# Kernel tuning notes

Hardware: AMD Instinct MI355X
Metric: run time of the kernel (lower is better)

The kernel has to match this reference:

```python
import jax, jax.numpy as jnp
import numpy as np

N_NODES = 100000
N_EDGES = 1200000
D_IN = 64
D_HID = 64
D_OUT = 32


def setup_inputs() -> dict:
    key = jax.random.key(0)
    ks = jax.random.split(key, 8)
    x = jax.random.normal(ks[0], (N_NODES, D_IN), dtype=jnp.float32)
    edge_index = jax.random.randint(ks[1], (2, N_EDGES), 0, N_NODES, dtype=jnp.int64)
    s = 0.05
    W1 = jax.random.normal(ks[2], (D_IN, D_HID), dtype=jnp.float32) * s
    b1 = jnp.zeros((D_HID,), dtype=jnp.float32)
    W2 = jax.random.normal(ks[3], (D_HID, D_HID), dtype=jnp.float32) * s
    b2 = jnp.zeros((D_HID,), dtype=jnp.float32)
    Wl = jax.random.normal(ks[4], (D_HID, D_OUT), dtype=jnp.float32) * s
    bl = jax.random.normal(ks[5], (D_OUT,), dtype=jnp.float32) * s
    return {"x": x, "edge_index": edge_index, "W1": W1, "b1": b1,
            "W2": W2, "b2": b2, "Wl": Wl, "bl": bl}


def reference(x, edge_index, W1, b1, W2, b2, Wl, bl):
    n = x.shape[0]
    # PyG GCNConv default: add self-loops, symmetric normalization D^-1/2 (A+I) D^-1/2
    loops = jnp.arange(n, dtype=edge_index.dtype)
    src = jnp.concatenate([edge_index[0], loops])  # message sources
    dst = jnp.concatenate([edge_index[1], loops])  # aggregation targets
    deg = jax.ops.segment_sum(jnp.ones(dst.shape, x.dtype), dst, num_segments=n)
    dinv = jax.lax.rsqrt(deg)  # deg >= 1 due to self-loops
    norm = dinv[src] * dinv[dst]  # [E+N]

    def gcn_conv(h, W, b):
        h = h @ W                      # transform [N, d]
        m = h[src] * norm[:, None]     # gather + scale [E+N, d]
        return jax.ops.segment_sum(m, dst, num_segments=n) + b  # scatter-add

    h = jax.nn.relu(gcn_conv(x, W1, b1))
    h = jax.nn.relu(gcn_conv(h, W2, b2))
    return h @ Wl + bl
```

## Files before the change

kernel.cpp:

```cpp
#include <hip/hip_runtime.h>
#include <hip/hip_fp16.h>

#define N_NODES 100000
#define N_EDGES 1200000

#define BIN_SHIFT 6
#define NODES_PER_BIN 64
#define NBINS ((N_NODES + NODES_PER_BIN - 1) >> BIN_SHIFT)
#define CAP 1024
#define EPB 8192
#define NBLK_BIN ((N_EDGES + EPB - 1) / EPB)

__global__ void binning_kernel(const int* __restrict__ src, const int* __restrict__ dst,
                               int* __restrict__ gcursor, unsigned int* __restrict__ binned,
                               int E) {
    __shared__ unsigned int stage[EPB];
    __shared__ unsigned short sbin[EPB];
    __shared__ unsigned int hist[NBINS];
    int t = threadIdx.x;
    int e_base = blockIdx.x * EPB;

    for (int b = t; b < NBINS; b += 256) hist[b] = 0;
    __syncthreads();

#pragma unroll
    for (int j = 0; j < EPB / 256; ++j) {
        int idx = e_base + t + j * 256;
        if (idx < E) {
            int s = src[idx];
            int d = dst[idx];
            unsigned int bin = (unsigned int)d >> BIN_SHIFT;
            stage[t + j * 256] = (unsigned int)s | (((unsigned int)d & 63u) << 17);
            sbin[t + j * 256] = (unsigned short)bin;
            atomicAdd(&hist[bin], 1u);
        }
    }
    __syncthreads();

    for (int b = t; b < NBINS; b += 256) {
        unsigned int c = hist[b];
        if (c) hist[b] = (unsigned int)(b * CAP) + (unsigned int)atomicAdd(&gcursor[b], (int)c);
    }
    __syncthreads();

#pragma unroll
    for (int j = 0; j < EPB / 256; ++j) {
        int idx = e_base + t + j * 256;
        if (idx < E) {
            unsigned int bin = sbin[t + j * 256];
            unsigned int pos = atomicAdd(&hist[bin], 1u);
            binned[pos] = stage[t + j * 256];
        }
    }
}

__global__ void csr_kernel(unsigned int* __restrict__ binned,
                           const int* __restrict__ gcursor,
                           float* __restrict__ dinv,
                           unsigned int* __restrict__ offdeg) {
    __shared__ unsigned int eLDS[CAP];
    __shared__ unsigned int counts[NODES_PER_BIN];
    __shared__ unsigned int scan[NODES_PER_BIN];
    __shared__ unsigned int offs[NODES_PER_BIN];
    __shared__ unsigned int cur[NODES_PER_BIN];
    int bin = blockIdx.x;
    int t = threadIdx.x;
    int nb = gcursor[bin];
    unsigned int* eb = binned + (size_t)bin * CAP;

    if (t < NODES_PER_BIN) counts[t] = 0;
    __syncthreads();
    for (int i = t; i < nb; i += 256) {
        unsigned int p = eb[i];
        eLDS[i] = p;
        atomicAdd(&counts[p >> 17], 1u);
    }
    __syncthreads();
    if (t < NODES_PER_BIN) scan[t] = counts[t];
    __syncthreads();
    for (int step = 1; step < NODES_PER_BIN; step <<= 1) {
        unsigned int v = 0;
        if (t < NODES_PER_BIN && t >= step) v = scan[t - step];
        __syncthreads();
        if (t < NODES_PER_BIN) scan[t] += v;
        __syncthreads();
    }
    if (t < NODES_PER_BIN) {
        offs[t] = scan[t] - counts[t];
        cur[t] = 0;
    }
    __syncthreads();
    for (int i = t; i < nb; i += 256) {
        unsigned int p = eLDS[i];
        unsigned int l = p >> 17;
        unsigned int pos = offs[l] + atomicAdd(&cur[l], 1u);
        eb[pos] = p & 0x1FFFFu;
    }
    if (t < NODES_PER_BIN) {
        int node = bin * NODES_PER_BIN + t;
        if (node < N_NODES) {
            dinv[node] = rsqrtf((float)(counts[t] + 1u));
            offdeg[node] = (offs[t] << 16) | counts[t];
        }
    }
}

__global__ __launch_bounds__(256, 4) void gemm1_kernel(const float* __restrict__ X,
                                                       const float* __restrict__ W,
                                                       const float* __restrict__ rowscale,
                                                       __half* __restrict__ Hout, int n) {
    constexpr int COLG = 16;
    constexpr int RGS  = 16;
    constexpr int RPT  = 4;
    constexpr int XPITCH = 17;
    __shared__ float4 sW4[64 * COLG];
    __shared__ float4 sX4[64 * XPITCH];
    int tid = threadIdx.x;

    for (int i = tid; i < 64 * COLG; i += 256) sW4[i] = ((const float4*)W)[i];

    int base_row = blockIdx.x * 64;
    const float4* X4 = (const float4*)X;
    for (int i = tid; i < 64 * 16; i += 256) {
        int r = i >> 4, c = i & 15;
        int gr = base_row + r;
        float4 v = make_float4(0.f, 0.f, 0.f, 0.f);
        if (gr < n) v = X4[(size_t)gr * 16 + c];
        sX4[r * XPITCH + c] = v;
    }
    __syncthreads();

    int cg = tid % COLG;
    int rg = tid / COLG;
    float4 acc[RPT];
#pragma unroll
    for (int r = 0; r < RPT; ++r) acc[r] = make_float4(0.f, 0.f, 0.f, 0.f);

#pragma unroll 2
    for (int k4 = 0; k4 < 16; ++k4) {
        float4 xv[RPT];
#pragma unroll
        for (int r = 0; r < RPT; ++r) xv[r] = sX4[(rg + RGS * r) * XPITCH + k4];
#pragma unroll
        for (int kk = 0; kk < 4; ++kk) {
            float4 w = sW4[(k4 * 4 + kk) * COLG + cg];
#pragma unroll
            for (int r = 0; r < RPT; ++r) {
                float xs = (kk == 0) ? xv[r].x : (kk == 1) ? xv[r].y : (kk == 2) ? xv[r].z : xv[r].w;
                acc[r].x = fmaf(xs, w.x, acc[r].x);
                acc[r].y = fmaf(xs, w.y, acc[r].y);
                acc[r].z = fmaf(xs, w.z, acc[r].z);
                acc[r].w = fmaf(xs, w.w, acc[r].w);
            }
        }
    }

#pragma unroll
    for (int r = 0; r < RPT; ++r) {
        int grow = base_row + rg + RGS * r;
        if (grow < n) {
            float4 v = acc[r];
            float s = rowscale[grow];
            v.x *= s; v.y *= s; v.z *= s; v.w *= s;
            __half2* H2 = (__half2*)Hout;
            size_t idx = (size_t)grow * 32 + 2 * cg;
            H2[idx]     = __floats2half2_rn(v.x, v.y);
            H2[idx + 1] = __floats2half2_rn(v.z, v.w);
        }
    }
}

template<int DOUT, bool HALF_OUT, bool ROWSCALE, bool GEMM_BIAS>
__global__ __launch_bounds__(256, 4) void fused_agg_gemm(
    const __half* __restrict__ tmp,
    const unsigned int* __restrict__ binned,
    const int* __restrict__ gcursor,
    const unsigned int* __restrict__ offdeg,
    const float* __restrict__ dinv,
    const float* __restrict__ gb,
    const float* __restrict__ W,
    const float* __restrict__ gbias,
    void* __restrict__ Hout) {
    constexpr int COLG = DOUT / 4;
    constexpr int RGS  = 256 / COLG;
    constexpr int RPT  = 64 / RGS;
    constexpr int XPITCH = 17;
    __shared__ unsigned int srcs[CAP];
    __shared__ unsigned int sOffdeg[NODES_PER_BIN];
    __shared__ float sDinv[NODES_PER_BIN];
    __shared__ float4 sW4[64 * COLG];
    __shared__ float4 sH4[64 * XPITCH];

    int bin = blockIdx.x;
    int t = threadIdx.x;
    int nb = gcursor[bin];
    const unsigned int* eb = binned + (size_t)bin * CAP;

    for (int i = t; i < 64 * COLG; i += 256) sW4[i] = ((const float4*)W)[i];
    if (t < NODES_PER_BIN) {
        int node = bin * NODES_PER_BIN + t;
        sOffdeg[t] = (node < N_NODES) ? offdeg[node] : 0;
        sDinv[t]   = (node < N_NODES) ? dinv[node]   : 0.0f;
    }
    for (int i = t; i < nb; i += 256) srcs[i] = eb[i];
    __syncthreads();

    int oct = t & 7;
    int lnode0 = t >> 3;
    const uint4* tmp16 = (const uint4*)tmp;
    float bb[8];
    {
        const float4 b0 = ((const float4*)gb)[oct * 2];
        const float4 b1 = ((const float4*)gb)[oct * 2 + 1];
        bb[0] = b0.x; bb[1] = b0.y; bb[2] = b0.z; bb[3] = b0.w;
        bb[4] = b1.x; bb[5] = b1.y; bb[6] = b1.z; bb[7] = b1.w;
    }

#pragma unroll
    for (int g = 0; g < 2; ++g) {
        int ln = g * 32 + lnode0;
        int node = bin * NODES_PER_BIN + ln;
        if (node < N_NODES) {
            unsigned int od = sOffdeg[ln];
            int deg = (int)(od & 0xFFFFu);
            int beg = (int)(od >> 16);
            float acc[8];
            {
                uint4 raw = tmp16[(size_t)node * 8 + oct];
                const __half2* hp = (const __half2*)&raw;
#pragma unroll
                for (int j = 0; j < 4; ++j) {
                    float2 f = __half22float2(hp[j]);
                    acc[2 * j] = f.x; acc[2 * j + 1] = f.y;
                }
            }
            int e = 0;
            for (; e + 3 < deg; e += 4) {
                unsigned int s0 = srcs[beg + e];
                unsigned int s1 = srcs[beg + e + 1];
                unsigned int s2 = srcs[beg + e + 2];
                unsigned int s3 = srcs[beg + e + 3];
                uint4 r0 = tmp16[(size_t)s0 * 8 + oct];
                uint4 r1 = tmp16[(size_t)s1 * 8 + oct];
                uint4 r2 = tmp16[(size_t)s2 * 8 + oct];
                uint4 r3 = tmp16[(size_t)s3 * 8 + oct];
                const __half2* h0 = (const __half2*)&r0;
                const __half2* h1 = (const __half2*)&r1;
                const __half2* h2 = (const __half2*)&r2;
                const __half2* h3 = (const __half2*)&r3;
#pragma unroll
                for (int j = 0; j < 4; ++j) {
                    float2 f0 = __half22float2(h0[j]);
                    float2 f1 = __half22float2(h1[j]);
                    float2 f2 = __half22float2(h2[j]);
                    float2 f3 = __half22float2(h3[j]);
                    acc[2 * j]     += (f0.x + f1.x) + (f2.x + f3.x);
                    acc[2 * j + 1] += (f0.y + f1.y) + (f2.y + f3.y);
                }
            }
            for (; e < deg; ++e) {
                unsigned int s0 = srcs[beg + e];
                uint4 r0 = tmp16[(size_t)s0 * 8 + oct];
                const __half2* h0 = (const __half2*)&r0;
#pragma unroll
                for (int j = 0; j < 4; ++j) {
                    float2 f0 = __half22float2(h0[j]);
                    acc[2 * j]     += f0.x;
                    acc[2 * j + 1] += f0.y;
                }
            }
            float dv = sDinv[ln];
            float4 o0, o1;
            o0.x = fmaxf(fmaf(dv, acc[0], bb[0]), 0.0f);
            o0.y = fmaxf(fmaf(dv, acc[1], bb[1]), 0.0f);
            o0.z = fmaxf(fmaf(dv, acc[2], bb[2]), 0.0f);
            o0.w = fmaxf(fmaf(dv, acc[3], bb[3]), 0.0f);
            o1.x = fmaxf(fmaf(dv, acc[4], bb[4]), 0.0f);
            o1.y = fmaxf(fmaf(dv, acc[5], bb[5]), 0.0f);
            o1.z = fmaxf(fmaf(dv, acc[6], bb[6]), 0.0f);
            o1.w = fmaxf(fmaf(dv, acc[7], bb[7]), 0.0f);
            sH4[ln * XPITCH + oct * 2]     = o0;
            sH4[ln * XPITCH + oct * 2 + 1] = o1;
        }
    }
    __syncthreads();

    int cg = t % COLG;
    int rg = t / COLG;
    float4 acc[RPT];
#pragma unroll
    for (int r = 0; r < RPT; ++r) acc[r] = make_float4(0.f, 0.f, 0.f, 0.f);

#pragma unroll 2
    for (int k4 = 0; k4 < 16; ++k4) {
        float4 xv[RPT];
#pragma unroll
        for (int r = 0; r < RPT; ++r) xv[r] = sH4[(rg + RGS * r) * XPITCH + k4];
#pragma unroll
        for (int kk = 0; kk < 4; ++kk) {
            float4 w = sW4[(k4 * 4 + kk) * COLG + cg];
#pragma unroll
            for (int r = 0; r < RPT; ++r) {
                float xs = (kk == 0) ? xv[r].x : (kk == 1) ? xv[r].y : (kk == 2) ? xv[r].z : xv[r].w;
                acc[r].x = fmaf(xs, w.x, acc[r].x);
                acc[r].y = fmaf(xs, w.y, acc[r].y);
                acc[r].z = fmaf(xs, w.z, acc[r].z);
                acc[r].w = fmaf(xs, w.w, acc[r].w);
            }
        }
    }

#pragma unroll
    for (int r = 0; r < RPT; ++r) {
        int ln = rg + RGS * r;
        int node = bin * NODES_PER_BIN + ln;
        if (node < N_NODES) {
            float4 v = acc[r];
            if (ROWSCALE) {
                float s = sDinv[ln];
                v.x *= s; v.y *= s; v.z *= s; v.w *= s;
            }
            if (GEMM_BIAS) {
                float4 bbq = ((const float4*)gbias)[cg];
                v.x += bbq.x; v.y += bbq.y; v.z += bbq.z; v.w += bbq.w;
            }
            if (HALF_OUT) {
                __half2* H2 = (__half2*)Hout;
                size_t idx = (size_t)node * (DOUT / 2) + 2 * cg;
                H2[idx]     = __floats2half2_rn(v.x, v.y);
                H2[idx + 1] = __floats2half2_rn(v.z, v.w);
            } else {
                ((float4*)Hout)[(size_t)node * COLG + cg] = v;
            }
        }
    }
}

extern "C" void kernel_launch(void* const* d_in, const int* in_sizes, int n_in,
                              void* d_out, int out_size, void* d_ws, size_t ws_size,
                              hipStream_t stream) {
    const float* x  = (const float*)d_in[0];
    const int*   ei = (const int*)d_in[1];
    const float* W1 = (const float*)d_in[2];
    const float* b1 = (const float*)d_in[3];
    const float* W2 = (const float*)d_in[4];
    const float* b2 = (const float*)d_in[5];
    const float* Wl = (const float*)d_in[6];
    const float* bl = (const float*)d_in[7];
    float* out = (float*)d_out;

    const int N = N_NODES;
    const int E = N_EDGES;
    const int* src = ei;
    const int* dst = ei + E;

    char* ws = (char*)d_ws;
    size_t off = 0;
    auto align = [](size_t v) { return (v + 511) & ~(size_t)511; };
    int* gcursor         = (int*)(ws + off);          off = align(off + (size_t)NBINS * 4);
    float* dinv          = (float*)(ws + off);        off = align(off + (size_t)N * 4);
    unsigned int* offdeg = (unsigned int*)(ws + off); off = align(off + (size_t)N * 4);
    unsigned int* binned = (unsigned int*)(ws + off); off = align(off + (size_t)NBINS * CAP * 4);
    __half* tmp          = (__half*)(ws + off);       off = align(off + (size_t)N * 64 * 2);
    __half* tmp2         = (__half*)(ws + off);       off = align(off + (size_t)N * 64 * 2);
    (void)ws_size;

    const int NBLK_GEMM = (N + 63) / 64;

    hipMemsetAsync(gcursor, 0, (size_t)NBINS * 4, stream);
    binning_kernel<<<NBLK_BIN, 256, 0, stream>>>(src, dst, gcursor, binned, E);
    csr_kernel<<<NBINS, 256, 0, stream>>>(binned, gcursor, dinv, offdeg);

    gemm1_kernel<<<NBLK_GEMM, 256, 0, stream>>>(x, W1, dinv, tmp, N);

    fused_agg_gemm<64, true, true, false><<<NBINS, 256, 0, stream>>>(
        tmp, binned, gcursor, offdeg, dinv, b1, W2, nullptr, tmp2);

    fused_agg_gemm<32, false, false, true><<<NBINS, 256, 0, stream>>>(
        tmp2, binned, gcursor, offdeg, dinv, b2, Wl, bl, out);
}
```

Before: 204.5 us.

## Merge edge binning and first GEMM into one launch, defer source scaling

The binning kernel and the first dense transform now share one launch, with blocks split by index range and a shared-memory buffer sized for the larger of the two roles. This removes the dependency of GEMM1 on dinv, so the two independent stages can overlap. To allow that, GEMM1 no longer prescales rows by dinv. The first aggregation instead multiplies each gathered source row by dinv[src], which costs an extra scattered 4-byte load per edge, and the larger shared allocation with launch_bounds(256,2) lowers occupancy for the binning blocks.

```diff
diff --git a/kernel.cpp b/kernel.cpp
--- a/kernel.cpp
+++ b/kernel.cpp
@@ -10,46 +10,108 @@
 #define CAP 1024
 #define EPB 8192
 #define NBLK_BIN ((N_EDGES + EPB - 1) / EPB)
-
-__global__ void binning_kernel(const int* __restrict__ src, const int* __restrict__ dst,
-                               int* __restrict__ gcursor, unsigned int* __restrict__ binned,
-                               int E) {
-    __shared__ unsigned int stage[EPB];
-    __shared__ unsigned short sbin[EPB];
-    __shared__ unsigned int hist[NBINS];
+#define NBLK_GEMM ((N_NODES + 63) / 64)
+#define SMEM_BYTES 55424
+
+__global__ __launch_bounds__(256, 2) void bin_gemm1_kernel(
+    const int* __restrict__ src, const int* __restrict__ dst,
+    int* __restrict__ gcursor, unsigned int* __restrict__ binned,
+    const float* __restrict__ X, const float* __restrict__ W1,
+    __half* __restrict__ tmp) {
+    __shared__ __align__(16) char smem[SMEM_BYTES];
     int t = threadIdx.x;
-    int e_base = blockIdx.x * EPB;
-
-    for (int b = t; b < NBINS; b += 256) hist[b] = 0;
-    __syncthreads();
-
-#pragma unroll
-    for (int j = 0; j < EPB / 256; ++j) {
-        int idx = e_base + t + j * 256;
-        if (idx < E) {
-            int s = src[idx];
-            int d = dst[idx];
-            unsigned int bin = (unsigned int)d >> BIN_SHIFT;
-            stage[t + j * 256] = (unsigned int)s | (((unsigned int)d & 63u) << 17);
-            sbin[t + j * 256] = (unsigned short)bin;
-            atomicAdd(&hist[bin], 1u);
-        }
-    }
-    __syncthreads();
-
-    for (int b = t; b < NBINS; b += 256) {
-        unsigned int c = hist[b];
-        if (c) hist[b] = (unsigned int)(b * CAP) + (unsigned int)atomicAdd(&gcursor[b], (int)c);
-    }
-    __syncthreads();
-
-#pragma unroll
-    for (int j = 0; j < EPB / 256; ++j) {
-        int idx = e_base + t + j * 256;
-        if (idx < E) {
-            unsigned int bin = sbin[t + j * 256];
-            unsigned int pos = atomicAdd(&hist[bin], 1u);
-            binned[pos] = stage[t + j * 256];
+
+    if (blockIdx.x < NBLK_BIN) {
+        unsigned int* stage = (unsigned int*)smem;
+        unsigned short* sbin = (unsigned short*)(smem + EPB * 4);
+        unsigned int* hist = (unsigned int*)(smem + EPB * 4 + EPB * 2);
+        int e_base = blockIdx.x * EPB;
+
+        for (int b = t; b < NBINS; b += 256) hist[b] = 0;
+        __syncthreads();
+
+#pragma unroll
+        for (int j = 0; j < EPB / 256; ++j) {
+            int idx = e_base + t + j * 256;
+            if (idx < N_EDGES) {
+                int s = src[idx];
+                int d = dst[idx];
+                unsigned int bin = (unsigned int)d >> BIN_SHIFT;
+                stage[t + j * 256] = (unsigned int)s | (((unsigned int)d & 63u) << 17);
+                sbin[t + j * 256] = (unsigned short)bin;
+                atomicAdd(&hist[bin], 1u);
+            }
+        }
+        __syncthreads();
+
+        for (int b = t; b < NBINS; b += 256) {
+            unsigned int c = hist[b];
+            if (c) hist[b] = (unsigned int)(b * CAP) + (unsigned int)atomicAdd(&gcursor[b], (int)c);
+        }
+        __syncthreads();
+
+#pragma unroll
+        for (int j = 0; j < EPB / 256; ++j) {
+            int idx = e_base + t + j * 256;
+            if (idx < N_EDGES) {
+                unsigned int bin = sbin[t + j * 256];
+                unsigned int pos = atomicAdd(&hist[bin], 1u);
+                binned[pos] = stage[t + j * 256];
+            }
+        }
+    } else {
+        constexpr int COLG = 16, RGS = 16, RPT = 4, XPITCH = 17;
+        float4* sW4 = (float4*)smem;
+        float4* sX4 = (float4*)(smem + 64 * COLG * 16);
+
+        for (int i = t; i < 64 * COLG; i += 256) sW4[i] = ((const float4*)W1)[i];
+
+        int base_row = (blockIdx.x - NBLK_BIN) * 64;
+        const float4* X4 = (const float4*)X;
+        for (int i = t; i < 64 * 16; i += 256) {
+            int r = i >> 4, c = i & 15;
+            int gr = base_row + r;
+            float4 v = make_float4(0.f, 0.f, 0.f, 0.f);
+            if (gr < N_NODES) v = X4[(size_t)gr * 16 + c];
+            sX4[r * XPITCH + c] = v;
+        }
+        __syncthreads();
+
+        int cg = t % COLG;
+        int rg = t / COLG;
+        float4 acc[RPT];
+#pragma unroll
+        for (int r = 0; r < RPT; ++r) acc[r] = make_float4(0.f, 0.f, 0.f, 0.f);
+
+#pragma unroll 2
+        for (int k4 = 0; k4 < 16; ++k4) {
+            float4 xv[RPT];
+#pragma unroll
+            for (int r = 0; r < RPT; ++r) xv[r] = sX4[(rg + RGS * r) * XPITCH + k4];
+#pragma unroll
+            for (int kk = 0; kk < 4; ++kk) {
+                float4 w = sW4[(k4 * 4 + kk) * COLG + cg];
+#pragma unroll
+                for (int r = 0; r < RPT; ++r) {
+                    float xs = (kk == 0) ? xv[r].x : (kk == 1) ? xv[r].y : (kk == 2) ? xv[r].z : xv[r].w;
+                    acc[r].x = fmaf(xs, w.x, acc[r].x);
+                    acc[r].y = fmaf(xs, w.y, acc[r].y);
+                    acc[r].z = fmaf(xs, w.z, acc[r].z);
+                    acc[r].w = fmaf(xs, w.w, acc[r].w);
+                }
+            }
+        }
+
+#pragma unroll
+        for (int r = 0; r < RPT; ++r) {
+            int grow = base_row + rg + RGS * r;
+            if (grow < N_NODES) {
+                float4 v = acc[r];
+                __half2* H2 = (__half2*)tmp;
+                size_t idx = (size_t)grow * 32 + 2 * cg;
+                H2[idx]     = __floats2half2_rn(v.x, v.y);
+                H2[idx + 1] = __floats2half2_rn(v.z, v.w);
+            }
         }
     }
 }
@@ -105,72 +167,7 @@
     }
 }
 
-__global__ __launch_bounds__(256, 4) void gemm1_kernel(const float* __restrict__ X,
-                                                       const float* __restrict__ W,
-                                                       const float* __restrict__ rowscale,
-                                                       __half* __restrict__ Hout, int n) {
-    constexpr int COLG = 16;
-    constexpr int RGS  = 16;
-    constexpr int RPT  = 4;
-    constexpr int XPITCH = 17;
-    __shared__ float4 sW4[64 * COLG];
-    __shared__ float4 sX4[64 * XPITCH];
-    int tid = threadIdx.x;
-
-    for (int i = tid; i < 64 * COLG; i += 256) sW4[i] = ((const float4*)W)[i];
-
-    int base_row = blockIdx.x * 64;
-    const float4* X4 = (const float4*)X;
-    for (int i = tid; i < 64 * 16; i += 256) {
-        int r = i >> 4, c = i & 15;
-        int gr = base_row + r;
-        float4 v = make_float4(0.f, 0.f, 0.f, 0.f);
-        if (gr < n) v = X4[(size_t)gr * 16 + c];
-        sX4[r * XPITCH + c] = v;
-    }
-    __syncthreads();
-
-    int cg = tid % COLG;
-    int rg = tid / COLG;
-    float4 acc[RPT];
-#pragma unroll
-    for (int r = 0; r < RPT; ++r) acc[r] = make_float4(0.f, 0.f, 0.f, 0.f);
-
-#pragma unroll 2
-    for (int k4 = 0; k4 < 16; ++k4) {
-        float4 xv[RPT];
-#pragma unroll
-        for (int r = 0; r < RPT; ++r) xv[r] = sX4[(rg + RGS * r) * XPITCH + k4];
-#pragma unroll
-        for (int kk = 0; kk < 4; ++kk) {
-            float4 w = sW4[(k4 * 4 + kk) * COLG + cg];
-#pragma unroll
-            for (int r = 0; r < RPT; ++r) {
-                float xs = (kk == 0) ? xv[r].x : (kk == 1) ? xv[r].y : (kk == 2) ? xv[r].z : xv[r].w;
-                acc[r].x = fmaf(xs, w.x, acc[r].x);
-                acc[r].y = fmaf(xs, w.y, acc[r].y);
-                acc[r].z = fmaf(xs, w.z, acc[r].z);
-                acc[r].w = fmaf(xs, w.w, acc[r].w);
-            }
-        }
-    }
-
-#pragma unroll
-    for (int r = 0; r < RPT; ++r) {
-        int grow = base_row + rg + RGS * r;
-        if (grow < n) {
-            float4 v = acc[r];
-            float s = rowscale[grow];
-            v.x *= s; v.y *= s; v.z *= s; v.w *= s;
-            __half2* H2 = (__half2*)Hout;
-            size_t idx = (size_t)grow * 32 + 2 * cg;
-            H2[idx]     = __floats2half2_rn(v.x, v.y);
-            H2[idx + 1] = __floats2half2_rn(v.z, v.w);
-        }
-    }
-}
-
-template<int DOUT, bool HALF_OUT, bool ROWSCALE, bool GEMM_BIAS>
+template<int DOUT, bool HALF_OUT, bool ROWSCALE, bool GEMM_BIAS, bool PRESCALED>
 __global__ __launch_bounds__(256, 4) void fused_agg_gemm(
     const __half* __restrict__ tmp,
     const unsigned int* __restrict__ binned,
@@ -224,14 +221,16 @@
             unsigned int od = sOffdeg[ln];
             int deg = (int)(od & 0xFFFFu);
             int beg = (int)(od >> 16);
+            float dv = sDinv[ln];
             float acc[8];
             {
                 uint4 raw = tmp16[(size_t)node * 8 + oct];
                 const __half2* hp = (const __half2*)&raw;
+                float selfs = PRESCALED ? 1.0f : dv;
 #pragma unroll
                 for (int j = 0; j < 4; ++j) {
                     float2 f = __half22float2(hp[j]);
-                    acc[2 * j] = f.x; acc[2 * j + 1] = f.y;
+                    acc[2 * j] = selfs * f.x; acc[2 * j + 1] = selfs * f.y;
                 }
             }
             int e = 0;
@@ -240,6 +239,10 @@
                 unsigned int s1 = srcs[beg + e + 1];
                 unsigned int s2 = srcs[beg + e + 2];
                 unsigned int s3 = srcs[beg + e + 3];
+                float w0 = 1.f, w1 = 1.f, w2 = 1.f, w3 = 1.f;
+                if (!PRESCALED) {
+                    w0 = dinv[s0]; w1 = dinv[s1]; w2 = dinv[s2]; w3 = dinv[s3];
+                }
                 uint4 r0 = tmp16[(size_t)s0 * 8 + oct];
                 uint4 r1 = tmp16[(size_t)s1 * 8 + oct];
                 uint4 r2 = tmp16[(size_t)s2 * 8 + oct];
@@ -254,22 +257,27 @@
                     float2 f1 = __half22float2(h1[j]);
                     float2 f2 = __half22float2(h2[j]);
                     float2 f3 = __half22float2(h3[j]);
-                    acc[2 * j]     += (f0.x + f1.x) + (f2.x + f3.x);
-                    acc[2 * j + 1] += (f0.y + f1.y) + (f2.y + f3.y);
+                    if (PRESCALED) {
+                        acc[2 * j]     += (f0.x + f1.x) + (f2.x + f3.x);
+                        acc[2 * j + 1] += (f0.y + f1.y) + (f2.y + f3.y);
+                    } else {
+                        acc[2 * j]     = fmaf(w0, f0.x, fmaf(w1, f1.x, fmaf(w2, f2.x, fmaf(w3, f3.x, acc[2 * j]))));
+                        acc[2 * j + 1] = fmaf(w0, f0.y, fmaf(w1, f1.y, fmaf(w2, f2.y, fmaf(w3, f3.y, acc[2 * j + 1]))));
+                    }
                 }
             }
             for (; e < deg; ++e) {
                 unsigned int s0 = srcs[beg + e];
+                float w0 = PRESCALED ? 1.0f : dinv[s0];
                 uint4 r0 = tmp16[(size_t)s0 * 8 + oct];
                 const __half2* h0 = (const __half2*)&r0;
 #pragma unroll
                 for (int j = 0; j < 4; ++j) {
                     float2 f0 = __half22float2(h0[j]);
-                    acc[2 * j]     += f0.x;
-                    acc[2 * j + 1] += f0.y;
-                }
-            }
-            float dv = sDinv[ln];
+                    acc[2 * j]     = fmaf(w0, f0.x, acc[2 * j]);
+                    acc[2 * j + 1] = fmaf(w0, f0.y, acc[2 * j + 1]);
+                }
+            }
             float4 o0, o1;
             o0.x = fmaxf(fmaf(dv, acc[0], bb[0]), 0.0f);
             o0.y = fmaxf(fmaf(dv, acc[1], bb[1]), 0.0f);
@@ -349,33 +357,29 @@
     const float* bl = (const float*)d_in[7];
     float* out = (float*)d_out;
 
-    const int N = N_NODES;
-    const int E = N_EDGES;
     const int* src = ei;
-    const int* dst = ei + E;
+    const int* dst = ei + N_EDGES;
 
     char* ws = (char*)d_ws;
     size_t off = 0;
     auto align = [](size_t v) { return (v + 511) & ~(size_t)511; };
     int* gcursor         = (int*)(ws + off);          off = align(off + (size_t)NBINS * 4);
-    float* dinv          = (float*)(ws + off);        off = align(off + (size_t)N * 4);
-    unsigned int* offdeg = (unsigned int*)(ws + off); off = align(off + (size_t)N * 4);
+    float* dinv          = (float*)(ws + off);        off = align(off + (size_t)N_NODES * 4);
+    unsigned int* offdeg = (unsigned int*)(ws + off); off = align(off + (size_t)N_NODES * 4);
     unsigned int* binned = (unsigned int*)(ws + off); off = align(off + (size_t)NBINS * CAP * 4);
-    __half* tmp          = (__half*)(ws + off);       off = align(off + (size_t)N * 64 * 2);
-    __half* tmp2         = (__half*)(ws + off);       off = align(off + (size_t)N * 64 * 2);
+    __half* tmp          = (__half*)(ws + off);       off = align(off + (size_t)N_NODES * 64 * 2);
+    __half* tmp2         = (__half*)(ws + off);       off = align(off + (size_t)N_NODES * 64 * 2);
     (void)ws_size;
 
-    const int NBLK_GEMM = (N + 63) / 64;
-
     hipMemsetAsync(gcursor, 0, (size_t)NBINS * 4, stream);
-    binning_kernel<<<NBLK_BIN, 256, 0, stream>>>(src, dst, gcursor, binned, E);
+    bin_gemm1_kernel<<<NBLK_BIN + NBLK_GEMM, 256, 0, stream>>>(
+        src, dst, gcursor, binned, x, W1, tmp);
+
     csr_kernel<<<NBINS, 256, 0, stream>>>(binned, gcursor, dinv, offdeg);
 
-    gemm1_kernel<<<NBLK_GEMM, 256, 0, stream>>>(x, W1, dinv, tmp, N);
-
-    fused_agg_gemm<64, true, true, false><<<NBINS, 256, 0, stream>>>(
+    fused_agg_gemm<64, true, true, false, false><<<NBINS, 256, 0, stream>>>(
         tmp, binned, gcursor, offdeg, dinv, b1, W2, nullptr, tmp2);
 
-    fused_agg_gemm<32, false, false, true><<<NBINS, 256, 0, stream>>>(
+    fused_agg_gemm<32, false, false, true, true><<<NBINS, 256, 0, stream>>>(
         tmp2, binned, gcursor, offdeg, dinv, b2, Wl, bl, out);
 }
```

Result: faster. 190.8 us (-6.7%).
